# Kernel optimization log

Measured on AMD Instinct MI355X. Metric: run time of the kernel, lower is better.

The kernel has to match this reference:

```python
import jax, jax.numpy as jnp
import numpy as np

BN_EPS = 1e-5

def _conv(x, w, b, pad):
    # x [B,C,H,W], w [O,I,kh,kw]
    y = jax.lax.conv_general_dilated(x, w, window_strides=(1, 1),
                                     padding=[(pad, pad), (pad, pad)],
                                     dimension_numbers=('NCHW', 'OIHW', 'NCHW'))
    return y + b[None, :, None, None]

def _bn(x, p):
    # p [4,C] rows: gamma, beta, running_mean, running_var (inference-mode BN)
    g, b, m, v = p
    scale = (g * jax.lax.rsqrt(v + BN_EPS))[None, :, None, None]
    return (x - m[None, :, None, None]) * scale + b[None, :, None, None]

def _up2_bilinear_ac(x):
    # UpsamplingBilinear2d(scale_factor=2) == bilinear, align_corners=True
    def interp(x, axis):
        n = x.shape[axis]
        out = 2 * n
        c = jnp.arange(out, dtype=x.dtype) * ((n - 1) / (out - 1))
        i0 = jnp.floor(c).astype(jnp.int32)
        i1 = jnp.minimum(i0 + 1, n - 1)
        w = c - i0.astype(x.dtype)
        sh = [1] * x.ndim
        sh[axis] = out
        w = w.reshape(sh)
        return jnp.take(x, i0, axis=axis) * (1 - w) + jnp.take(x, i1, axis=axis) * w
    return interp(interp(x, 2), 3)

def _dilate(x, k, iterations):
    # cv2.dilate with ones(k,k) kernel == sliding-window max (the custom-kernel target);
    # get_open_map detaches, hence stop_gradient.
    for _ in range(iterations):
        x = jax.lax.reduce_window(x, -jnp.inf, jax.lax.max,
                                  (1, 1, k, k), (1, 1, 1, 1), 'SAME')
    return jax.lax.stop_gradient(x)

def _pixel_shuffle2(x):
    B, C4, H, W = x.shape
    C = C4 // 4
    x = x.reshape(B, C, 2, 2, H, W).transpose(0, 1, 4, 2, 5, 3)
    return x.reshape(B, C, 2 * H, 2 * W)

def setup_inputs() -> dict:
    key = jax.random.key(0)
    ks = jax.random.split(key, 16)
    B, C1, C2, H, W = 8, 64, 128, 64, 64

    def bn_params(k, C):
        k1, k2, k3, k4 = jax.random.split(k, 4)
        g = jax.random.uniform(k1, (C,)) * 0.5 + 0.75
        b = jax.random.normal(k2, (C,)) * 0.1
        m = jax.random.normal(k3, (C,)) * 0.1
        v = jax.random.uniform(k4, (C,)) + 0.5
        return jnp.stack([g, b, m, v])

    def conv_w(k, o, i, kk):
        return jax.random.normal(k, (o, i, kk, kk)) * 0.05

    return {
        'cur_x': jax.random.normal(ks[0], (B, C1, 2 * H, 2 * W)),
        'dep_x': jax.random.normal(ks[1], (B, C2, H, W)),
        'in_map': jax.random.normal(ks[2], (B, 1, H, W)),
        'up_w': conv_w(ks[3], 4 * C1, C2, 7), 'up_b': jnp.zeros((4 * C1,)),
        'up_bn': bn_params(ks[4], 4 * C1),
        'conv2_w': conv_w(ks[5], C1, C1, 3), 'conv2_b': jnp.zeros((C1,)),
        'd1_w': conv_w(ks[6], C1, C1, 3), 'd1_b': jnp.zeros((C1,)),
        'd1_bn': bn_params(ks[7], C1),
        'd2_w': conv_w(ks[8], C1, C1, 3), 'd2_b': jnp.zeros((C1,)),
        'd2_bn': bn_params(ks[9], C1),
        'd3_w': conv_w(ks[10], C1, C1, 3), 'd3_b': jnp.zeros((C1,)),
        'd3_bn': bn_params(ks[11], C1),
        'out_w': conv_w(ks[12], 1, C1, 7), 'out_b': jnp.zeros((1,)),
        'beta': jnp.ones((1,)),
    }

def reference(cur_x, dep_x, in_map, up_w, up_b, up_bn, conv2_w, conv2_b,
              d1_w, d1_b, d1_bn, d2_w, d2_b, d2_bn, d3_w, d3_b, d3_bn,
              out_w, out_b, beta):
    K, IT = 3, 1  # opr_kernel_size, iterations
    # up + pixel shuffle: [B,C2,H,W] -> [B,C1,2H,2W]
    dep = _pixel_shuffle2(jax.nn.relu(_bn(_conv(dep_x, up_w, up_b, 3), up_bn)))
    in_map1 = 1.0 - in_map
    input_map = jax.nn.sigmoid(_up2_bilinear_ac(in_map))
    input_map1 = jax.nn.sigmoid(_up2_bilinear_ac(in_map1))
    increase_map = _dilate(input_map, K, IT) - input_map
    increase_map1 = _dilate(increase_map, K, IT) - increase_map
    increase_map2 = _dilate(input_map1, K, IT) - input_map1
    outmap = increase_map + increase_map1 + increase_map2
    fn = _conv(outmap * cur_x, conv2_w, conv2_b, 1)
    r = jax.nn.relu(_bn(_conv(dep + beta * fn, d1_w, d1_b, 1), d1_bn))
    r = jax.nn.relu(_bn(_conv(r, d2_w, d2_b, 1), d2_bn))
    r = jax.nn.relu(_bn(_conv(r, d3_w, d3_b, 1), d3_bn))
    output_map = _conv(r, out_w, out_b, 3)
    return (r, output_map)
```

## Files before the change

### kernel.cpp

```cpp
#include <hip/hip_runtime.h>
#include <hip/hip_bf16.h>
#include <math.h>

static __device__ __forceinline__ float sigm(float x) { return 1.0f / (1.0f + expf(-x)); }

static __device__ __forceinline__ short f2bf_s(float f) {
    unsigned u = __float_as_uint(f);
    u += 0x7fffu + ((u >> 16) & 1u);
    return (short)(u >> 16);
}
static __device__ __forceinline__ float bfb2f(short s) {
    return __uint_as_float(((unsigned)(unsigned short)s) << 16);
}

typedef __attribute__((ext_vector_type(8))) short short8;
typedef __attribute__((ext_vector_type(4))) short short4v;
typedef __attribute__((ext_vector_type(4))) float f32x4;

static __device__ __forceinline__ void gl_lds16(const void* g, void* l) {
    __builtin_amdgcn_global_load_lds(
        (const __attribute__((address_space(1))) unsigned int*)g,
        (__attribute__((address_space(3))) unsigned int*)l, 16, 0, 0);
}

__global__ __launch_bounds__(256) void k_prep_all(
    const float* __restrict__ in_map, short* __restrict__ om_bf,
    const float* __restrict__ w0, const float* __restrict__ w1,
    const float* __restrict__ w2, const float* __restrict__ w3,
    short* __restrict__ wb3,
    const float* __restrict__ up_w, short* __restrict__ wb,
    const float* __restrict__ dep_x, short* __restrict__ px) {
    __shared__ float s_u[20][20];
    __shared__ float s_inc[18][18];
    int blk = blockIdx.x;
    int tid = threadIdx.x;

    if (blk < 512) {
        int b = blk >> 6;
        int inner = blk & 63;
        int ty0 = (inner >> 3) << 4, tx0 = (inner & 7) << 4;
        const float* p = in_map + (b << 12);
        const float s = 63.0f / 127.0f;
        for (int e = tid; e < 400; e += 256) {
            int yy = e / 20, xx = e % 20;
            int gy = ty0 + yy - 2, gx = tx0 + xx - 2;
            float v = 0.0f;
            if ((unsigned)gy < 128u && (unsigned)gx < 128u) {
                float cy = gy * s, cx = gx * s;
                int iy0 = (int)cy, ix0 = (int)cx;
                float wy = cy - (float)iy0, wx = cx - (float)ix0;
                int iy1 = min(iy0 + 1, 63), ix1 = min(ix0 + 1, 63);
                float v00 = p[(iy0 << 6) + ix0], v01 = p[(iy0 << 6) + ix1];
                float v10 = p[(iy1 << 6) + ix0], v11 = p[(iy1 << 6) + ix1];
                v = (1.0f - wy) * ((1.0f - wx) * v00 + wx * v01) +
                    wy          * ((1.0f - wx) * v10 + wx * v11);
            }
            s_u[yy][xx] = v;
        }
        __syncthreads();
        for (int e = tid; e < 324; e += 256) {
            int yy = e / 18, xx = e % 18;
            int gy = ty0 + yy - 1, gx = tx0 + xx - 1;
            float val = -INFINITY;
            if ((unsigned)gy < 128u && (unsigned)gx < 128u) {
                float uc = s_u[yy + 1][xx + 1];
                float mx = -INFINITY;
                for (int dy = -1; dy <= 1; ++dy) {
                    int ny = gy + dy; if ((unsigned)ny >= 128u) continue;
                    for (int dx = -1; dx <= 1; ++dx) {
                        int nx = gx + dx; if ((unsigned)nx >= 128u) continue;
                        mx = fmaxf(mx, s_u[yy + 1 + dy][xx + 1 + dx]);
                    }
                }
                val = sigm(mx) - sigm(uc);
            }
            s_inc[yy][xx] = val;
        }
        __syncthreads();
        int row = tid >> 4, col = tid & 15;
        int gy = ty0 + row, gx = tx0 + col;
        float mx = -INFINITY;
        #pragma unroll
        for (int dy = 0; dy < 3; ++dy)
            #pragma unroll
            for (int dx = 0; dx < 3; ++dx)
                mx = fmaxf(mx, s_inc[row + dy][col + dx]);
        float uc = s_u[row + 2][col + 2];
        float mn = INFINITY;
        for (int dy = -1; dy <= 1; ++dy) {
            int ny = gy + dy; if ((unsigned)ny >= 128u) continue;
            for (int dx = -1; dx <= 1; ++dx) {
                int nx = gx + dx; if ((unsigned)nx >= 128u) continue;
                mn = fminf(mn, s_u[row + 2 + dy][col + 2 + dx]);
            }
        }
        float inc2 = sigm(1.0f - mn) - sigm(1.0f - uc);
        om_bf[(b << 14) + (gy << 7) + gx] = f2bf_s(mx + inc2);
    } else if (blk < 1088) {
        int s = (blk - 512) * 256 + tid;
        int layer = s / 36864; int r = s - layer * 36864;
        const float* w = (layer == 0) ? w0 : (layer == 1) ? w1 : (layer == 2) ? w2 : w3;
        int o = r / 576; int rem = r - o * 576;
        int c = rem / 9; int t = rem - c * 9;
        int dy = t / 3, dx = t - dy * 3;
        int cc = c >> 5, cl = c & 31;
        wb3[layer * 36864 + (((cc * 3 + dx) * 3 + dy) * 64 + o) * 32 + cl] = f2bf_s(w[r]);
    } else if (blk < 7360) {
        int s = (blk - 1088) * 256 + tid;
        int O = s / 6272; int r = s - O * 6272;
        int C = r / 49;   int T = r - C * 49;
        int dy = T / 7, dx = T - dy * 7;
        int nt = O >> 6, o = O & 63;
        int cc = C >> 5, c = C & 31;
        int W = ((((nt * 4 + cc) * 7 + dx) * 7 + dy) * 64 + o) * 32 + c;
        wb[W] = f2bf_s(up_w[s]);
    } else {
        int idx = blk - 7360;
        int b = idx / 70, yp = idx - (idx / 70) * 70;
        int y = yp - 3;
        bool inY = (unsigned)y < 64u;
        for (int cc = 0; cc < 4; ++cc) {
            short* orow = px + (((long)(b * 4 + cc) * 70 + yp) * 70) * 40;
            for (int e = tid; e < 350; e += 256) {
                int p2 = e / 70, xp = e - p2 * 70;
                int xg = xp - 3;
                short8 v = (short8){0, 0, 0, 0, 0, 0, 0, 0};
                if (p2 < 4 && inY && (unsigned)xg < 64u) {
                    const float* src = dep_x + (((b * 128 + cc * 32 + p2 * 8) << 12)) + (y << 6) + xg;
                    #pragma unroll
                    for (int i = 0; i < 8; ++i) v[i] = f2bf_s(src[i << 12]);
                }
                *(short8*)&orow[xp * 40 + p2 * 8] = v;
            }
        }
    }
}

__global__ __launch_bounds__(256) void k_premult(const float* __restrict__ cur_x,
                                                 const short* __restrict__ om_bf,
                                                 short* __restrict__ xin2) {
    int e = blockIdx.x * 256 + threadIdx.x;
    int flat = e << 2;
    int pix = flat & 16383;
    int b = flat >> 20;
    f32x4 xv = *(const f32x4*)&cur_x[flat];
    short4v ov = *(const short4v*)&om_bf[(b << 14) + pix];
    short4v res;
    #pragma unroll
    for (int k = 0; k < 4; ++k) res[k] = f2bf_s(xv[k] * bfb2f(ov[k]));
    *(short4v*)&xin2[flat] = res;
}

__global__ __launch_bounds__(512, 4) void k_upconv_mfma(
    const short* __restrict__ px,
    const short* __restrict__ wb,
    const float* __restrict__ cb,
    const float* __restrict__ bnp,
    short* __restrict__ dep) {
    __shared__ __attribute__((aligned(16))) short s_in[19360];
    int tid = threadIdx.x;
    int wave = tid >> 6, lane = tid & 63;
    int q = lane >> 4, m = lane & 15;
    int mw = wave & 3, ng = wave >> 2;
    int ty0 = (blockIdx.x >> 2) * 16;
    int tx0 = (blockIdx.x & 3) * 16;
    int nt = blockIdx.y;
    int b = blockIdx.z;
    f32x4 acc[4][2];
    #pragma unroll
    for (int i = 0; i < 4; ++i)
        #pragma unroll
        for (int j = 0; j < 2; ++j)
            acc[i][j] = (f32x4){0.f, 0.f, 0.f, 0.f};

    auto stage = [&](int cc) {
        const short* pxcc = px + ((((long)(b * 4 + cc) * 70 + ty0) * 70 + tx0) * 40);
        for (int c0 = (wave << 6); c0 < 2420; c0 += 512) {
            int chunk = c0 + lane;
            int row = chunk / 110;
            int k = chunk - row * 110;
            if (chunk < 2420)
                gl_lds16(pxcc + row * 2800 + (k << 3), &s_in[c0 << 3]);
        }
    };

    for (int cc = 0; cc < 4; ++cc) {
        if (cc) __syncthreads();
        stage(cc);
        __syncthreads();
        const short* sb = &s_in[0];
        const short* wcc = wb + ((nt * 4 + cc) * 49) * 2048;
        #pragma unroll 1
        for (int dx = 0; dx < 7; ++dx) {
            short8 a10[10];
            #pragma unroll
            for (int r = 0; r < 10; ++r)
                a10[r] = *(const short8*)&sb[((mw * 4 + r) * 22 + m + dx) * 40 + q * 8];
            const short* wdx = wcc + ((dx * 7) << 11);
            short8 wf[7];
            #pragma unroll
            for (int dy = 0; dy < 7; ++dy)
                wf[dy] = *(const short8*)(wdx + (dy << 11) + ((ng * 32 + m) << 5) + (q << 3));
            #pragma unroll
            for (int dy = 0; dy < 7; ++dy)
                #pragma unroll
                for (int i = 0; i < 4; ++i)
                    acc[i][0] = __builtin_amdgcn_mfma_f32_16x16x32_bf16(
                        a10[i + dy], wf[dy], acc[i][0], 0, 0, 0);
            #pragma unroll
            for (int dy = 0; dy < 7; ++dy)
                wf[dy] = *(const short8*)(wdx + (dy << 11) + ((ng * 32 + 16 + m) << 5) + (q << 3));
            #pragma unroll
            for (int dy = 0; dy < 7; ++dy)
                #pragma unroll
                for (int i = 0; i < 4; ++i)
                    acc[i][1] = __builtin_amdgcn_mfma_f32_16x16x32_bf16(
                        a10[i + dy], wf[dy], acc[i][1], 0, 0, 0);
        }
    }
    #pragma unroll
    for (int j = 0; j < 2; ++j) {
        int o = nt * 64 + ng * 32 + j * 16 + m;
        float g  = bnp[o],       bt = bnp[256 + o];
        float mn = bnp[512 + o], vv = bnp[768 + o];
        float scale = g * rsqrtf(vv + 1e-5f);
        float cbf = cb[o];
        int c = o >> 2, sbit = (o >> 1) & 1, tbit = o & 1;
        #pragma unroll
        for (int i = 0; i < 4; ++i) {
            int y = ty0 + mw * 4 + i;
            #pragma unroll
            for (int reg = 0; reg < 4; ++reg) {
                int xc = tx0 + q * 4 + reg;
                float val = (acc[i][j][reg] + cbf - mn) * scale + bt;
                val = fmaxf(val, 0.0f);
                dep[((b * 64 + c) << 14) + ((2 * y + sbit) << 7) + (2 * xc + tbit)] = f2bf_s(val);
            }
        }
    }
}

template <int MODE, bool OUTBF>
__global__ __launch_bounds__(512, 4) void k_conv3m(
    const short* __restrict__ xin,
    const short* __restrict__ wl,
    const short* __restrict__ dep,
    const float* __restrict__ cb,
    const float* __restrict__ bnp,
    const float* __restrict__ beta,
    void* __restrict__ out) {
    __shared__ __attribute__((aligned(16))) short s_in[324 * 88];
    int tid = threadIdx.x;
    int wave = tid >> 6, lane = tid & 63;
    int q = lane >> 4, m = lane & 15;
    int mw = wave & 3, og = wave >> 2;
    int ty0 = (blockIdx.x >> 3) * 16;
    int tx0 = (blockIdx.x & 7) * 16;
    int b = blockIdx.z;
    f32x4 acc[4][2];
    #pragma unroll
    for (int i = 0; i < 4; ++i)
        #pragma unroll
        for (int j = 0; j < 2; ++j)
            acc[i][j] = (f32x4){0.f, 0.f, 0.f, 0.f};
    const short* xb = xin + ((long)(b * 64) << 14);
    for (int e = tid; e < 864; e += 512) {
        int cq = e / 108; int rem = e - cq * 108;
        int yy = rem / 6; int g = rem - yy * 6;
        int gy = ty0 + yy - 1;
        int gx0 = tx0 - 4 + (g << 2);
        short4v v[8];
        if ((unsigned)gy < 128u && (unsigned)gx0 < 128u) {
            const short* src = xb + ((cq * 8) << 14) + (gy << 7) + gx0;
            #pragma unroll
            for (int j2 = 0; j2 < 8; ++j2) v[j2] = *(const short4v*)(src + (j2 << 14));
        } else {
            #pragma unroll
            for (int j2 = 0; j2 < 8; ++j2) v[j2] = (short4v){0, 0, 0, 0};
        }
        #pragma unroll
        for (int t = 0; t < 4; ++t) {
            int xx = (g << 2) - 3 + t;
            if ((unsigned)xx < 18u) {
                short8 pk;
                #pragma unroll
                for (int j2 = 0; j2 < 8; ++j2) pk[j2] = v[j2][t];
                *(short8*)&s_in[(yy * 18 + xx) * 88 + cq * 8] = pk;
            }
        }
    }
    __syncthreads();
    #pragma unroll 1
    for (int cc = 0; cc < 2; ++cc) {
        #pragma unroll 1
        for (int dx = 0; dx < 3; ++dx) {
            short8 a6[6];
            #pragma unroll
            for (int r = 0; r < 6; ++r)
                a6[r] = *(const short8*)&s_in[((mw * 4 + r) * 18 + m + dx) * 88 + cc * 32 + q * 8];
            const short* wdx = wl + (((cc * 3 + dx) * 3) << 11);
            short8 wf[3];
            #pragma unroll
            for (int dy = 0; dy < 3; ++dy)
                wf[dy] = *(const short8*)(wdx + (dy << 11) + ((og * 32 + m) << 5) + (q << 3));
            #pragma unroll
            for (int dy = 0; dy < 3; ++dy)
                #pragma unroll
                for (int i = 0; i < 4; ++i)
                    acc[i][0] = __builtin_amdgcn_mfma_f32_16x16x32_bf16(
                        a6[i + dy], wf[dy], acc[i][0], 0, 0, 0);
            #pragma unroll
            for (int dy = 0; dy < 3; ++dy)
                wf[dy] = *(const short8*)(wdx + (dy << 11) + ((og * 32 + 16 + m) << 5) + (q << 3));
            #pragma unroll
            for (int dy = 0; dy < 3; ++dy)
                #pragma unroll
                for (int i = 0; i < 4; ++i)
                    acc[i][1] = __builtin_amdgcn_mfma_f32_16x16x32_bf16(
                        a6[i + dy], wf[dy], acc[i][1], 0, 0, 0);
        }
    }
    float betav = (MODE == 1) ? beta[0] : 0.0f;
    #pragma unroll
    for (int j = 0; j < 2; ++j) {
        int o = og * 32 + j * 16 + m;
        float cbf = cb[o];
        float scale = 1.0f, shift = 0.0f;
        if (MODE == 0) {
            float g  = bnp[o],       bt = bnp[64 + o];
            float mm = bnp[128 + o], vv = bnp[192 + o];
            scale = g * rsqrtf(vv + 1e-5f);
            shift = bt - mm * scale;
        }
        #pragma unroll
        for (int i = 0; i < 4; ++i) {
            int y = ty0 + mw * 4 + i;
            int base = ((b * 64 + o) << 14) + (y << 7) + tx0 + q * 4;
            float vals[4];
            if (MODE == 1) {
                short4v dv = *(const short4v*)&dep[base];
                #pragma unroll
                for (int reg = 0; reg < 4; ++reg)
                    vals[reg] = bfb2f(dv[reg]) + betav * (acc[i][j][reg] + cbf);
            } else {
                #pragma unroll
                for (int reg = 0; reg < 4; ++reg)
                    vals[reg] = fmaxf((acc[i][j][reg] + cbf) * scale + shift, 0.0f);
            }
            if (OUTBF) {
                short4v sv;
                #pragma unroll
                for (int reg = 0; reg < 4; ++reg) sv[reg] = f2bf_s(vals[reg]);
                *(short4v*)((short*)out + base) = sv;
            } else {
                f32x4 fv;
                #pragma unroll
                for (int reg = 0; reg < 4; ++reg) fv[reg] = vals[reg];
                *(f32x4*)((float*)out + base) = fv;
            }
        }
    }
}

__global__ __launch_bounds__(256) void k_outconv(
    const float* __restrict__ r,
    const float* __restrict__ w,
    const float* __restrict__ ob,
    float* __restrict__ out) {
    __shared__ float s_in[8][22][22];
    int tid = threadIdx.x;
    int ty = tid >> 4, tx = tid & 15;
    int ty0 = (blockIdx.x >> 3) << 4, tx0 = (blockIdx.x & 7) << 4;
    int b = blockIdx.z;
    float acc4[4] = {0.f, 0.f, 0.f, 0.f};
    for (int c0 = 0; c0 < 64; c0 += 8) {
        __syncthreads();
        for (int e = tid; e < 8 * 484; e += 256) {
            int i = e / 484; int r2 = e - i * 484; int yy = r2 / 22; int xx = r2 - yy * 22;
            int gy = ty0 + yy - 3, gx = tx0 + xx - 3;
            float v = 0.0f;
            if ((unsigned)gy < 128u && (unsigned)gx < 128u)
                v = r[((b * 64 + c0 + i) << 14) + (gy << 7) + gx];
            s_in[i][yy][xx] = v;
        }
        __syncthreads();
        for (int i = 0; i < 8; ++i) {
            const float* wrow = w + (c0 + i) * 49;
            #pragma unroll
            for (int dy = 0; dy < 7; ++dy)
                #pragma unroll
                for (int dx = 0; dx < 7; ++dx)
                    acc4[i & 3] = fmaf(s_in[i][ty + dy][tx + dx], wrow[dy * 7 + dx], acc4[i & 3]);
        }
    }
    out[(b << 14) + ((ty0 + ty) << 7) + tx0 + tx] =
        (acc4[0] + acc4[1]) + (acc4[2] + acc4[3]) + ob[0];
}

extern "C" void kernel_launch(void* const* d_in, const int* in_sizes, int n_in,
                              void* d_out, int out_size, void* d_ws, size_t ws_size,
                              hipStream_t stream) {
    const float* cur_x  = (const float*)d_in[0];
    const float* dep_x  = (const float*)d_in[1];
    const float* in_map = (const float*)d_in[2];
    const float* up_w   = (const float*)d_in[3];
    const float* up_b   = (const float*)d_in[4];
    const float* up_bn  = (const float*)d_in[5];
    const float* c2_w   = (const float*)d_in[6];
    const float* c2_b   = (const float*)d_in[7];
    const float* d1_w   = (const float*)d_in[8];
    const float* d1_b   = (const float*)d_in[9];
    const float* d1_bn  = (const float*)d_in[10];
    const float* d2_w   = (const float*)d_in[11];
    const float* d2_b   = (const float*)d_in[12];
    const float* d2_bn  = (const float*)d_in[13];
    const float* d3_w   = (const float*)d_in[14];
    const float* d3_b   = (const float*)d_in[15];
    const float* d3_bn  = (const float*)d_in[16];
    const float* out_w  = (const float*)d_in[17];
    const float* out_b  = (const float*)d_in[18];
    const float* beta   = (const float*)d_in[19];

    char* ob = (char*)d_out;
    float* r_out  = (float*)ob;
    short* A      = (short*)d_ws;
    short* B      = (short*)ob;
    short* C      = (short*)(ob + 16777216);
    short* wb     = C;
    short* px     = wb + 1605632;
    short* om_bf  = (short*)(ob + 32532480);
    short* wb3    = (short*)(ob + 33554432);
    float* mapout = (float*)(ob + 33554432);

    k_prep_all<<<7920, 256, 0, stream>>>(in_map, om_bf, c2_w, d1_w, d2_w, d3_w, wb3,
                                         up_w, wb, dep_x, px);
    k_premult<<<8192, 256, 0, stream>>>(cur_x, om_bf, A);
    k_upconv_mfma<<<dim3(16, 4, 8), 512, 0, stream>>>(px, wb, up_b, up_bn, B);
    k_conv3m<1, true><<<dim3(64, 1, 8), 512, 0, stream>>>(
        A, wb3 + 0 * 36864, B, c2_b, nullptr, beta, C);
    k_conv3m<0, true><<<dim3(64, 1, 8), 512, 0, stream>>>(
        C, wb3 + 1 * 36864, nullptr, d1_b, d1_bn, nullptr, B);
    k_conv3m<0, true><<<dim3(64, 1, 8), 512, 0, stream>>>(
        B, wb3 + 2 * 36864, nullptr, d2_b, d2_bn, nullptr, A);
    k_conv3m<0, false><<<dim3(64, 1, 8), 512, 0, stream>>>(
        A, wb3 + 3 * 36864, nullptr, d3_b, d3_bn, nullptr, r_out);
    k_outconv<<<dim3(64, 1, 8), 256, 0, stream>>>(r_out, out_w, out_b, mapout);
}
```

Before: 463.8 us.

## Switch intermediate activations to channel-blocked cell layout for conv tiles

```diff
diff --git a/kernel.cpp b/kernel.cpp
--- a/kernel.cpp
+++ b/kernel.cpp
@@ -136,19 +136,25 @@
     }
 }
 
-__global__ __launch_bounds__(256) void k_premult(const float* __restrict__ cur_x,
-                                                 const short* __restrict__ om_bf,
-                                                 short* __restrict__ xin2) {
-    int e = blockIdx.x * 256 + threadIdx.x;
-    int flat = e << 2;
-    int pix = flat & 16383;
-    int b = flat >> 20;
-    f32x4 xv = *(const f32x4*)&cur_x[flat];
-    short4v ov = *(const short4v*)&om_bf[(b << 14) + pix];
-    short4v res;
-    #pragma unroll
-    for (int k = 0; k < 4; ++k) res[k] = f2bf_s(xv[k] * bfb2f(ov[k]));
-    *(short4v*)&xin2[flat] = res;
+__global__ __launch_bounds__(256) void k_premult_cell(
+    const float* __restrict__ cur_x,
+    const short* __restrict__ om_bf,
+    short* __restrict__ xcell) {
+    int y = blockIdx.x;
+    int cc = blockIdx.y;
+    int b = blockIdx.z;
+    int tid = threadIdx.x;
+    int x = tid >> 1, p2 = tid & 1;
+    float om = bfb2f(om_bf[(b << 14) + (y << 7) + x]);
+    const float* src = cur_x + (((b * 64 + cc * 32 + p2 * 16) << 14) + (y << 7) + x);
+    short8 v0, v1;
+    #pragma unroll
+    for (int i = 0; i < 8; ++i) v0[i] = f2bf_s(src[(long)i << 14] * om);
+    #pragma unroll
+    for (int i = 0; i < 8; ++i) v1[i] = f2bf_s(src[(long)(8 + i) << 14] * om);
+    short* dst = xcell + ((((long)(b * 2 + cc) * 128 + y) * 128 + x) << 5) + (p2 << 4);
+    *(short8*)dst = v0;
+    *(short8*)(dst + 8) = v1;
 }
 
 __global__ __launch_bounds__(512, 4) void k_upconv_mfma(
@@ -156,7 +162,7 @@
     const short* __restrict__ wb,
     const float* __restrict__ cb,
     const float* __restrict__ bnp,
-    short* __restrict__ dep) {
+    short* __restrict__ depc) {
     __shared__ __attribute__((aligned(16))) short s_in[19360];
     int tid = threadIdx.x;
     int wave = tid >> 6, lane = tid & 63;
@@ -226,15 +232,18 @@
         float scale = g * rsqrtf(vv + 1e-5f);
         float cbf = cb[o];
         int c = o >> 2, sbit = (o >> 1) & 1, tbit = o & 1;
+        int cc2 = c >> 5, slot = c & 31;
         #pragma unroll
         for (int i = 0; i < 4; ++i) {
             int y = ty0 + mw * 4 + i;
+            int Y = 2 * y + sbit;
             #pragma unroll
             for (int reg = 0; reg < 4; ++reg) {
                 int xc = tx0 + q * 4 + reg;
+                int X = 2 * xc + tbit;
                 float val = (acc[i][j][reg] + cbf - mn) * scale + bt;
                 val = fmaxf(val, 0.0f);
-                dep[((b * 64 + c) << 14) + ((2 * y + sbit) << 7) + (2 * xc + tbit)] = f2bf_s(val);
+                depc[((((long)(b * 2 + cc2) * 128 + Y) * 128 + X) << 5) + slot] = f2bf_s(val);
             }
         }
     }
@@ -242,14 +251,14 @@
 
 template <int MODE, bool OUTBF>
 __global__ __launch_bounds__(512, 4) void k_conv3m(
-    const short* __restrict__ xin,
+    const short* __restrict__ xcell,
     const short* __restrict__ wl,
-    const short* __restrict__ dep,
+    const short* __restrict__ depc,
     const float* __restrict__ cb,
     const float* __restrict__ bnp,
     const float* __restrict__ beta,
     void* __restrict__ out) {
-    __shared__ __attribute__((aligned(16))) short s_in[324 * 88];
+    __shared__ __attribute__((aligned(16))) short s_in[20736];
     int tid = threadIdx.x;
     int wave = tid >> 6, lane = tid & 63;
     int q = lane >> 4, m = lane & 15;
@@ -263,31 +272,16 @@
         #pragma unroll
         for (int j = 0; j < 2; ++j)
             acc[i][j] = (f32x4){0.f, 0.f, 0.f, 0.f};
-    const short* xb = xin + ((long)(b * 64) << 14);
-    for (int e = tid; e < 864; e += 512) {
-        int cq = e / 108; int rem = e - cq * 108;
-        int yy = rem / 6; int g = rem - yy * 6;
-        int gy = ty0 + yy - 1;
-        int gx0 = tx0 - 4 + (g << 2);
-        short4v v[8];
-        if ((unsigned)gy < 128u && (unsigned)gx0 < 128u) {
-            const short* src = xb + ((cq * 8) << 14) + (gy << 7) + gx0;
-            #pragma unroll
-            for (int j2 = 0; j2 < 8; ++j2) v[j2] = *(const short4v*)(src + (j2 << 14));
-        } else {
-            #pragma unroll
-            for (int j2 = 0; j2 < 8; ++j2) v[j2] = (short4v){0, 0, 0, 0};
-        }
-        #pragma unroll
-        for (int t = 0; t < 4; ++t) {
-            int xx = (g << 2) - 3 + t;
-            if ((unsigned)xx < 18u) {
-                short8 pk;
-                #pragma unroll
-                for (int j2 = 0; j2 < 8; ++j2) pk[j2] = v[j2][t];
-                *(short8*)&s_in[(yy * 18 + xx) * 88 + cq * 8] = pk;
-            }
-        }
+    for (int chunk = tid; chunk < 2592; chunk += 512) {
+        int cc = chunk / 1296;
+        int rem = chunk - cc * 1296;
+        int cell = rem >> 2, part = rem & 3;
+        int Y = cell / 18, X = cell - Y * 18;
+        int gy = ty0 + Y - 1, gx = tx0 + X - 1;
+        short8 v = (short8){0, 0, 0, 0, 0, 0, 0, 0};
+        if ((unsigned)gy < 128u && (unsigned)gx < 128u)
+            v = *(const short8*)(xcell + ((((long)(b * 2 + cc) * 128 + gy) * 128 + gx) << 5) + (part << 3));
+        *(short8*)&s_in[chunk << 3] = v;
     }
     __syncthreads();
     #pragma unroll 1
@@ -297,7 +291,7 @@
             short8 a6[6];
             #pragma unroll
             for (int r = 0; r < 6; ++r)
-                a6[r] = *(const short8*)&s_in[((mw * 4 + r) * 18 + m + dx) * 88 + cc * 32 + q * 8];
+                a6[r] = *(const short8*)&s_in[((cc * 324 + (mw * 4 + r) * 18 + m + dx) << 5) + q * 8];
             const short* wdx = wl + (((cc * 3 + dx) * 3) << 11);
             short8 wf[3];
             #pragma unroll
@@ -335,28 +329,21 @@
         #pragma unroll
         for (int i = 0; i < 4; ++i) {
             int y = ty0 + mw * 4 + i;
-            int base = ((b * 64 + o) << 14) + (y << 7) + tx0 + q * 4;
-            float vals[4];
-            if (MODE == 1) {
-                short4v dv = *(const short4v*)&dep[base];
-                #pragma unroll
-                for (int reg = 0; reg < 4; ++reg)
-                    vals[reg] = bfb2f(dv[reg]) + betav * (acc[i][j][reg] + cbf);
-            } else {
-                #pragma unroll
-                for (int reg = 0; reg < 4; ++reg)
-                    vals[reg] = fmaxf((acc[i][j][reg] + cbf) * scale + shift, 0.0f);
-            }
-            if (OUTBF) {
-                short4v sv;
-                #pragma unroll
-                for (int reg = 0; reg < 4; ++reg) sv[reg] = f2bf_s(vals[reg]);
-                *(short4v*)((short*)out + base) = sv;
-            } else {
-                f32x4 fv;
-                #pragma unroll
-                for (int reg = 0; reg < 4; ++reg) fv[reg] = vals[reg];
-                *(f32x4*)((float*)out + base) = fv;
+            #pragma unroll
+            for (int reg = 0; reg < 4; ++reg) {
+                int xpos = tx0 + q * 4 + reg;
+                long caddr = ((((long)(b * 2 + og) * 128 + y) * 128 + xpos) << 5) + j * 16 + m;
+                float val;
+                if (MODE == 1) {
+                    val = bfb2f(depc[caddr]) + betav * (acc[i][j][reg] + cbf);
+                } else {
+                    val = fmaxf((acc[i][j][reg] + cbf) * scale + shift, 0.0f);
+                }
+                if (OUTBF) {
+                    ((short*)out)[caddr] = f2bf_s(val);
+                } else {
+                    ((float*)out)[((b * 64 + o) << 14) + (y << 7) + xpos] = val;
+                }
             }
         }
     }
@@ -434,7 +421,7 @@
 
     k_prep_all<<<7920, 256, 0, stream>>>(in_map, om_bf, c2_w, d1_w, d2_w, d3_w, wb3,
                                          up_w, wb, dep_x, px);
-    k_premult<<<8192, 256, 0, stream>>>(cur_x, om_bf, A);
+    k_premult_cell<<<dim3(128, 2, 8), 256, 0, stream>>>(cur_x, om_bf, A);
     k_upconv_mfma<<<dim3(16, 4, 8), 512, 0, stream>>>(px, wb, up_b, up_bn, B);
     k_conv3m<1, true><<<dim3(64, 1, 8), 512, 0, stream>>>(
         A, wb3 + 0 * 36864, B, c2_b, nullptr, beta, C);
```

Result: faster. 426.4 us (-8.1%).
